# Performance work log

Hardware: AMD Instinct MI355X
Metric: run time of the kernel (lower is better)

## Reference

```python
import jax, jax.numpy as jnp
import numpy as np

B, C, D, H, W = 4, 256, 16, 16, 16


def setup_inputs() -> dict:
    key = jax.random.key(0)
    ks = jax.random.split(key, 9)
    s = 1.0 / np.sqrt(C)
    inp = {
        "x": jax.random.normal(ks[0], (B, C, D, H, W), dtype=jnp.float32),
        "wq": jax.random.normal(ks[1], (C, C), dtype=jnp.float32) * s,
        "bq": jax.random.normal(ks[2], (C,), dtype=jnp.float32) * 0.02,
        "wk": jax.random.normal(ks[3], (C, C), dtype=jnp.float32) * s,
        "bk": jax.random.normal(ks[4], (C,), dtype=jnp.float32) * 0.02,
        "wv": jax.random.normal(ks[5], (C, C), dtype=jnp.float32) * s,
        "bv": jax.random.normal(ks[6], (C,), dtype=jnp.float32) * 0.02,
        "wp": jax.random.normal(ks[7], (C, C), dtype=jnp.float32) * s,
        "bp": jax.random.normal(ks[8], (C,), dtype=jnp.float32) * 0.02,
    }
    return inp


def reference(x, wq, bq, wk, bk, wv, bv, wp, bp):
    b, c, d, h, w = x.shape
    xf = x.reshape(b, c, d * h * w)  # (B, C, N)
    # 1x1 Conv3d == per-voxel linear map over channels
    q = jnp.einsum('oc,bcn->bon', wq, xf) + bq[:, None]
    k = jnp.einsum('oc,bcn->bon', wk, xf) + bk[:, None]
    v = jnp.einsum('oc,bcn->bon', wv, xf) + bv[:, None]
    # scores[b,i,j] = q[:, :, i] . k[:, :, j], scaled AFTER the bmm (as in source)
    scores = jnp.einsum('bci,bcj->bij', q, k) * (c ** -0.5)
    p = jax.nn.softmax(scores, axis=2)  # (B, N, N), softmax over keys j
    # attention[b,c,i] = sum_j v[b,c,j] * p[b,i,j]
    attn = jnp.einsum('bcj,bij->bci', v, p)
    out = jnp.einsum('oc,bcn->bon', wp, attn) + bp[:, None]
    return x + out.reshape(b, c, d, h, w)
```

## Files before the change

kernel.cpp:

```cpp
#include <hip/hip_runtime.h>

typedef unsigned short u16;
typedef unsigned int u32;
typedef __bf16 v8bf __attribute__((ext_vector_type(8)));
typedef float v4f __attribute__((ext_vector_type(4)));

#define DEV __device__ __forceinline__

constexpr int CB = 4;
constexpr int C = 256;
constexpr int NN = 4096;
constexpr float LOG2E = 1.4426950408889634f;
constexpr int PST = 44;

DEV u16 f2bf(float f) {
  union { float f; u32 u; } v; v.f = f;
  u32 r = v.u + 0x7fffu + ((v.u >> 16) & 1u);
  return (u16)(r >> 16);
}
DEV float bf2f(u16 h) {
  union { u32 u; float f; } v; v.u = ((u32)h) << 16; return v.f;
}

DEV void dma16(const u16* g, const u16* lds_base) {
  __builtin_amdgcn_global_load_lds(
      (const __attribute__((address_space(1))) void*)(unsigned long long)g,
      (__attribute__((address_space(3))) void*)(u32)(unsigned long long)lds_base,
      16, 0, 0);
}

__global__ __launch_bounds__(256) void k_transpose(const float* __restrict__ x,
                                                   u16* __restrict__ xT) {
  __shared__ float tile[32][33];
  int b = blockIdx.z;
  int n0 = blockIdx.x * 32, c0 = blockIdx.y * 32;
  int tx = threadIdx.x & 31, ty = threadIdx.x >> 5;
  const float* xb = x + (long)b * C * NN;
#pragma unroll
  for (int r = 0; r < 4; ++r)
    tile[ty + r * 8][tx] = xb[(long)(c0 + ty + r * 8) * NN + n0 + tx];
  __syncthreads();
  u16* xTb = xT + (long)b * NN * C;
#pragma unroll
  for (int r = 0; r < 4; ++r)
    xTb[(long)(n0 + ty + r * 8) * C + c0 + tx] = f2bf(tile[tx][ty + r * 8]);
}

__global__ __launch_bounds__(256) void k_cvt4(const float* __restrict__ s0,
                                              const float* __restrict__ s1,
                                              const float* __restrict__ s2,
                                              const float* __restrict__ s3,
                                              u16* __restrict__ d0, u16* __restrict__ d1,
                                              u16* __restrict__ d2, u16* __restrict__ d3,
                                              float* __restrict__ Mbuf) {
  if (blockIdx.x == 0 && blockIdx.y == 0 && threadIdx.x < 8) Mbuf[threadIdx.x] = 0.f;
  int wsel = blockIdx.y;
  const float* s = wsel == 0 ? s0 : wsel == 1 ? s1 : wsel == 2 ? s2 : s3;
  u16* d = wsel == 0 ? d0 : wsel == 1 ? d1 : wsel == 2 ? d2 : d3;
  int i = blockIdx.x * 256 + threadIdx.x;
  d[i] = f2bf(s[i]);
}

DEV void stage_dma(const u16* __restrict__ g, const u16* lds, int w, int lane) {
#pragma unroll
  for (int i = 0; i < 8; ++i) {
    int idx = w * 8 + i;
    int r = idx * 2 + (lane >> 5);
    int cg = (lane & 31) ^ (r & 7);
    dma16(g + (long)r * 256 + cg * 8, lds + idx * 512);
  }
}

__global__ __launch_bounds__(256) void k_qkv(
    const u16* __restrict__ xT, const u16* __restrict__ wqb, const u16* __restrict__ wkb,
    const u16* __restrict__ wvb, const float* __restrict__ bq, const float* __restrict__ bk,
    const float* __restrict__ bv, u16* __restrict__ qO, u16* __restrict__ kO,
    u16* __restrict__ vO) {
  __shared__ __align__(16) u16 Ash[64 * 256];
  __shared__ __align__(16) u16 Bsh[64 * 256];
  int t = threadIdx.x, w = t >> 6, lane = t & 63, lr = lane & 15, q = lane >> 4;
  int m0 = blockIdx.x * 64, n0 = blockIdx.y * 64, b = blockIdx.z;
  const int xk = lr & 7;
  stage_dma(xT + (long)b * NN * C + (long)m0 * 256, Ash, w, lane);
  stage_dma(wqb + (long)n0 * 256, Bsh, w, lane);
  asm volatile("s_waitcnt vmcnt(0)\n\ts_barrier" ::: "memory");
#pragma unroll 1
  for (int wsel = 0; wsel < 3; ++wsel) {
    v4f acc[4];
#pragma unroll
    for (int nt = 0; nt < 4; ++nt)
#pragma unroll
      for (int r = 0; r < 4; ++r) acc[nt][r] = 0.f;
#pragma unroll
    for (int ks = 0; ks < 8; ++ks) {
      int cg = ((ks * 4 + q) ^ xk) << 3;
      v8bf a = *reinterpret_cast<const v8bf*>(Ash + (w * 16 + lr) * 256 + cg);
#pragma unroll
      for (int nt = 0; nt < 4; ++nt) {
        v8bf bb = *reinterpret_cast<const v8bf*>(Bsh + (nt * 16 + lr) * 256 + cg);
        acc[nt] = __builtin_amdgcn_mfma_f32_16x16x32_bf16(a, bb, acc[nt], 0, 0, 0);
      }
    }
    asm volatile("s_waitcnt lgkmcnt(0)\n\ts_barrier" ::: "memory");
    if (wsel < 2) {
      stage_dma((wsel == 0 ? wkb : wvb) + (long)n0 * 256, Bsh, w, lane);
      const float* bias = wsel == 0 ? bq : bk;
#pragma unroll
      for (int nt = 0; nt < 4; ++nt) {
#pragma unroll
        for (int r = 0; r < 4; ++r) {
          int gm = m0 + w * 16 + q * 4 + r;
          int gn = n0 + nt * 16 + lr;
          float val = acc[nt][r] + bias[gn];
          if (wsel == 0) {
            qO[((long)b * NN + gm) * C + gn] = f2bf(val * (0.0625f * LOG2E));
          } else {
            kO[((long)b * NN + gm) * C + gn] = f2bf(val);
          }
        }
      }
      asm volatile("s_waitcnt vmcnt(0)\n\ts_barrier" ::: "memory");
    } else {
      u16* Vt = Ash;
#pragma unroll
      for (int nt = 0; nt < 4; ++nt) {
#pragma unroll
        for (int r = 0; r < 4; ++r) {
          int gn_l = nt * 16 + lr;
          int gm_l = w * 16 + q * 4 + r;
          float val = acc[nt][r] + bv[n0 + gn_l];
          Vt[gn_l * 72 + gm_l] = f2bf(val);
        }
      }
      asm volatile("s_waitcnt lgkmcnt(0)\n\ts_barrier" ::: "memory");
      int row = t >> 2;
      u16* vrow = vO + (long)b * C * NN + (long)(n0 + row) * NN + m0;
#pragma unroll
      for (int s2 = 0; s2 < 2; ++s2) {
        int seg = (t & 3) * 2 + s2;
        *reinterpret_cast<uint4*>(vrow + seg * 8) =
            *reinterpret_cast<const uint4*>(Vt + row * 72 + seg * 8);
      }
    }
  }
}

__global__ __launch_bounds__(256) void k_maxnorm(const u16* __restrict__ qT,
                                                 const u16* __restrict__ kT,
                                                 float* __restrict__ Mbuf) {
  int b = blockIdx.z, tsel = blockIdx.y;
  const u16* src = (tsel ? kT : qT) + (long)b * NN * C;
  int row = blockIdx.x * 64 + (threadIdx.x >> 2);
  const uint4* pp =
      reinterpret_cast<const uint4*>(src + (long)row * C + (threadIdx.x & 3) * 64);
  float s = 0.f;
#pragma unroll
  for (int u = 0; u < 8; ++u) {
    uint4 d = pp[u];
    const u16* e = reinterpret_cast<const u16*>(&d);
#pragma unroll
    for (int i = 0; i < 8; ++i) { float f = bf2f(e[i]); s += f * f; }
  }
  s += __shfl_xor(s, 1, 64);
  s += __shfl_xor(s, 2, 64);
#pragma unroll
  for (int d2 = 4; d2 < 64; d2 <<= 1) s = fmaxf(s, __shfl_xor(s, d2, 64));
  if ((threadIdx.x & 63) == 0)
    atomicMax((u32*)(Mbuf + tsel * 4 + b), __float_as_uint(s));
}

__global__ __launch_bounds__(256) void k_gemm(
    const u16* __restrict__ A, long aStr, const u16* __restrict__ Bm, long bStr,
    const float* __restrict__ biasM, const float* __restrict__ biasN,
    const float* __restrict__ resid, long rStr, float scale,
    float* __restrict__ outF, u16* __restrict__ outH, long oStr, int ldm, int ldn) {
  __shared__ __align__(16) u16 Ash[64 * 256];
  __shared__ __align__(16) u16 Bsh[64 * 256];
  int t = threadIdx.x;
  int w = t >> 6, lane = t & 63, lr = lane & 15, q = lane >> 4;
  int m0 = blockIdx.x * 64, n0 = blockIdx.y * 64, b = blockIdx.z;
  const int xk = lr & 7;
  stage_dma(A + b * aStr + (long)m0 * 256, Ash, w, lane);
  stage_dma(Bm + b * bStr + (long)n0 * 256, Bsh, w, lane);
  asm volatile("s_waitcnt vmcnt(0)\n\ts_barrier" ::: "memory");
  v4f acc[4];
#pragma unroll
  for (int nt = 0; nt < 4; ++nt)
#pragma unroll
    for (int r = 0; r < 4; ++r) acc[nt][r] = 0.f;
#pragma unroll
  for (int ks = 0; ks < 8; ++ks) {
    int cg = ((ks * 4 + q) ^ xk) << 3;
    v8bf a = *reinterpret_cast<const v8bf*>(Ash + (w * 16 + lr) * 256 + cg);
#pragma unroll
    for (int nt = 0; nt < 4; ++nt) {
      v8bf bb = *reinterpret_cast<const v8bf*>(Bsh + (nt * 16 + lr) * 256 + cg);
      acc[nt] = __builtin_amdgcn_mfma_f32_16x16x32_bf16(a, bb, acc[nt], 0, 0, 0);
    }
  }
#pragma unroll
  for (int nt = 0; nt < 4; ++nt) {
#pragma unroll
    for (int r = 0; r < 4; ++r) {
      int gm = m0 + w * 16 + q * 4 + r;
      int gn = n0 + nt * 16 + lr;
      float val = acc[nt][r];
      if (biasM) val += biasM[gm];
      if (biasN) val += biasN[gn];
      val *= scale;
      long addr = b * oStr + (long)gm * ldm + (long)gn * ldn;
      if (resid) val += resid[b * rStr + (long)gm * ldm + (long)gn * ldn];
      if (outF) outF[addr] = val;
      else outH[addr] = f2bf(val);
    }
  }
}

DEV void flash_issue(const u16* kb, const u16* vb, const u16* kshb, const u16* vshb,
                     int j0, int w, int lane) {
#pragma unroll
  for (int i = 0; i < 4; ++i) {
    int idx = w * 4 + i;
    int kr = idx * 2 + (lane >> 5);
    int kc = (lane & 31) ^ (kr & 7);
    dma16(kb + (long)(j0 + kr) * 256 + kc * 8, kshb + idx * 512);
  }
#pragma unroll
  for (int i = 0; i < 4; ++i) {
    int idx = w * 4 + i;
    int vr = idx * 16 + (lane >> 2);
    int vc = (lane & 3) ^ ((vr ^ (vr >> 2)) & 3);
    dma16(vb + (long)vr * NN + j0 + vc * 8, vshb + idx * 512);
  }
}

__global__ __launch_bounds__(256, 2) void k_flash(const u16* __restrict__ qT,
                                                  const u16* __restrict__ kT,
                                                  const u16* __restrict__ V,
                                                  u16* __restrict__ op0,
                                                  u16* __restrict__ op1,
                                                  u16* __restrict__ op2,
                                                  u16* __restrict__ op3,
                                                  float* __restrict__ ml,
                                                  const float* __restrict__ Mbuf,
                                                  int span) {
  __shared__ __align__(16) u16 ksh[2][32 * 256];
  __shared__ __align__(16) u16 vsh[2][256 * 32];
  __shared__ __align__(16) u16 psh[64 * PST];
  int t = threadIdx.x;
  int w = t >> 6, lane = t & 63, lr = lane & 15, q = lane >> 4;
  int b = blockIdx.z, h = blockIdx.y;
  int i0 = blockIdx.x * 64;
  const u16* qb = qT + ((long)b * NN + i0 + w * 16) * C;
  const u16* kb = kT + (long)b * NN * C;
  const u16* vb = V + (long)b * C * NN;
  float M = sqrtf(Mbuf[b] * Mbuf[4 + b]) + 1.0f;

  v8bf qf[8];
#pragma unroll
  for (int ks = 0; ks < 8; ++ks)
    qf[ks] = *reinterpret_cast<const v8bf*>(qb + lr * C + ks * 32 + q * 8);

  v4f accO[16];
#pragma unroll
  for (int ct = 0; ct < 16; ++ct)
#pragma unroll
    for (int r = 0; r < 4; ++r) accO[ct][r] = 0.f;
  float lsum[4] = {0.f, 0.f, 0.f, 0.f};

  u16* pw = psh + w * 16 * PST;
  const int xk = lr & 7;
  const int xv = (lr ^ (lr >> 2)) & 3;

  int jstart = h * span;
  int niter = span >> 5;
  flash_issue(kb, vb, ksh[0], vsh[0], jstart, w, lane);
  int cur = 0;
#pragma unroll 1
  for (int it = 0; it < niter; ++it) {
    int j0 = jstart + (it << 5);
    int jn = (it + 1 < niter) ? j0 + 32 : jstart;
    asm volatile("s_waitcnt lgkmcnt(0)\n\ts_barrier" ::: "memory");
    flash_issue(kb, vb, ksh[cur ^ 1], vsh[cur ^ 1], jn, w, lane);
    asm volatile("s_waitcnt vmcnt(8)\n\ts_barrier" ::: "memory");

    const u16* kcur = ksh[cur];
    const u16* vcur = vsh[cur];
    v4f s[2];
#pragma unroll
    for (int jt = 0; jt < 2; ++jt)
#pragma unroll
      for (int r = 0; r < 4; ++r) s[jt][r] = 0.f;
#pragma unroll
    for (int ks = 0; ks < 8; ++ks) {
#pragma unroll
      for (int jt = 0; jt < 2; ++jt) {
        v8bf kf = *reinterpret_cast<const v8bf*>(
            kcur + (jt * 16 + lr) * 256 + (((ks * 4 + q) ^ xk) << 3));
        s[jt] = __builtin_amdgcn_mfma_f32_16x16x32_bf16(qf[ks], kf, s[jt], 0, 0, 0);
      }
    }

#pragma unroll
    for (int jt = 0; jt < 2; ++jt) {
#pragma unroll
      for (int r = 0; r < 4; ++r) {
        float p = exp2f(s[jt][r] - M);
        lsum[r] += p;
        u32 pb = (__float_as_uint(p) + 0x8000u) >> 16;
        pw[(q * 4 + r) * PST + jt * 16 + lr] = (u16)pb;
      }
    }
    asm volatile("s_waitcnt lgkmcnt(0)\n\ts_barrier" ::: "memory");
    v8bf pa[4];
#pragma unroll
    for (int qs = 0; qs < 4; ++qs)
      pa[qs] = *reinterpret_cast<const v8bf*>(psh + (qs * 16 + lr) * PST + q * 8);
    const u16* vwp = vcur + w * 64 * 32;
#pragma unroll
    for (int cs = 0; cs < 4; ++cs) {
      v8bf v0 = *reinterpret_cast<const v8bf*>(
          vwp + (cs * 16 + lr) * 32 + ((q ^ xv) << 3));
#pragma unroll
      for (int qs = 0; qs < 4; ++qs)
        accO[qs * 4 + cs] =
            __builtin_amdgcn_mfma_f32_16x16x32_bf16(pa[qs], v0, accO[qs * 4 + cs], 0, 0, 0);
    }
    cur ^= 1;
  }

#pragma unroll
  for (int r = 0; r < 4; ++r) {
#pragma unroll
    for (int d = 1; d < 16; d <<= 1) lsum[r] += __shfl_xor(lsum[r], d, 64);
  }
  u16* opp = h == 0 ? op0 : h == 1 ? op1 : h == 2 ? op2 : op3;
  u16* ob = opp + ((long)b * NN + i0) * C;
#pragma unroll
  for (int qs = 0; qs < 4; ++qs)
#pragma unroll
    for (int cs = 0; cs < 4; ++cs)
#pragma unroll
      for (int r = 0; r < 4; ++r)
        ob[(qs * 16 + q * 4 + r) * C + w * 64 + cs * 16 + lr] =
            f2bf(accO[qs * 4 + cs][r]);
  if (lr == 0) {
    long rbase = ((long)h * CB + b) * NN + i0 + w * 16 + q * 4;
#pragma unroll
    for (int r = 0; r < 4; ++r) {
      ml[(rbase + r) * 2] = M;
      ml[(rbase + r) * 2 + 1] = lsum[r];
    }
  }
}

__global__ __launch_bounds__(256) void k_combine(const u16* __restrict__ p0,
                                                 const u16* __restrict__ p1,
                                                 const u16* __restrict__ p2,
                                                 const u16* __restrict__ p3,
                                                 const float* __restrict__ ml,
                                                 u16* __restrict__ o, int js) {
  long row = (long)blockIdx.x * 8 + (threadIdx.x >> 5);
  int tc = (threadIdx.x & 31) * 8;
  float m[4], l[4];
  float mx = -3.0e38f;
  for (int h = 0; h < js; ++h) {
    m[h] = ml[((long)h * CB * NN + row) * 2];
    l[h] = ml[((long)h * CB * NN + row) * 2 + 1];
    mx = fmaxf(mx, m[h]);
  }
  float tot = 0.f, a[4];
  for (int h = 0; h < js; ++h) { a[h] = exp2f(m[h] - mx); tot += a[h] * l[h]; }
  float inv = 1.f / tot;
  float acc[8];
#pragma unroll
  for (int i = 0; i < 8; ++i) acc[i] = 0.f;
  const u16* ps[4] = {p0, p1, p2, p3};
  for (int h = 0; h < js; ++h) {
    uint4 u = *reinterpret_cast<const uint4*>(ps[h] + row * C + tc);
    const u16* p = reinterpret_cast<const u16*>(&u);
    float wgt = a[h] * inv;
#pragma unroll
    for (int i = 0; i < 8; ++i) acc[i] += wgt * bf2f(p[i]);
  }
  u16 outv[8];
#pragma unroll
  for (int i = 0; i < 8; ++i) outv[i] = f2bf(acc[i]);
  *reinterpret_cast<uint4*>(o + row * C + tc) = *reinterpret_cast<const uint4*>(outv);
}

extern "C" void kernel_launch(void* const* d_in, const int* in_sizes, int n_in,
                              void* d_out, int out_size, void* d_ws, size_t ws_size,
                              hipStream_t stream) {
  const float* x = (const float*)d_in[0];
  const float* wq = (const float*)d_in[1];
  const float* bq = (const float*)d_in[2];
  const float* wk = (const float*)d_in[3];
  const float* bk = (const float*)d_in[4];
  const float* wv = (const float*)d_in[5];
  const float* bv = (const float*)d_in[6];
  const float* wp = (const float*)d_in[7];
  const float* bp = (const float*)d_in[8];
  float* out = (float*)d_out;
  char* ws = (char*)d_ws;

  const long SLOT = 8388608L;
  const size_t NEED4 = 524288UL + 7 * 8388608UL + 524288UL + 4096UL;
  int js = (ws_size >= NEED4) ? 4 : 2;

  u16* wqb = (u16*)(ws + 0);
  u16* wkb = (u16*)(ws + 131072L);
  u16* wvb = (u16*)(ws + 262144L);
  u16* wpb = (u16*)(ws + 393216L);
  char* base = ws + 524288L;
  u16* xT  = (u16*)(base);
  u16* qTw = (u16*)(base + 1 * SLOT);
  u16* kTw = (u16*)(base + 2 * SLOT);
  u16* vw  = (u16*)(base + 3 * SLOT);
  u16* op1 = (u16*)(base + 4 * SLOT);
  u16* op2 = js == 4 ? (u16*)(base + 5 * SLOT) : op1;
  u16* op3 = js == 4 ? (u16*)(base + 6 * SLOT) : op1;
  float* ml = (float*)(base + (js == 4 ? 7 : 5) * SLOT);
  float* Mbuf = ml + 131072;
  u16* op0 = xT;
  u16* oW  = qTw;

  k_cvt4<<<dim3(256, 4), 256, 0, stream>>>(wq, wk, wv, wp, wqb, wkb, wvb, wpb, Mbuf);
  k_transpose<<<dim3(128, 8, CB), 256, 0, stream>>>(x, xT);
  k_qkv<<<dim3(64, 4, CB), 256, 0, stream>>>(xT, wqb, wkb, wvb, bq, bk, bv, qTw, kTw, vw);
  k_maxnorm<<<dim3(64, 2, CB), 256, 0, stream>>>(qTw, kTw, Mbuf);
  k_flash<<<dim3(64, js, CB), 256, 0, stream>>>(qTw, kTw, vw, op0, op1, op2, op3, ml,
                                                Mbuf, NN / js);
  k_combine<<<2048, 256, 0, stream>>>(op0, op1, op2, op3, ml, oW, js);

  long nc = (long)NN * C;
  k_gemm<<<dim3(4, 64, CB), 256, 0, stream>>>(wpb, 0, oW, nc, bp, nullptr, x, nc,
                                              1.0f, out, nullptr, nc, NN, 1);
}
```

Baseline: 265.0 us.

## Software-pipeline flash loop: V in registers, double-buffered P, one barrier per step

Restructures the attention inner loop so V tiles are loaded directly from global memory into registers instead of staged through LDS. P is double-buffered in shared memory so the PV MFMA for iteration it-1 overlaps with the QK and softmax of iteration it. Only one barrier remains per step, and the loop is manually unrolled by two to alternate buffers. This cuts LDS traffic and synchronisation, but raises register pressure and relies on an even iteration count.

```diff
diff --git a/kernel.cpp b/kernel.cpp
--- a/kernel.cpp
+++ b/kernel.cpp
@@ -216,8 +216,7 @@
   }
 }
 
-DEV void flash_issue(const u16* kb, const u16* vb, const u16* kshb, const u16* vshb,
-                     int j0, int w, int lane) {
+DEV void kissue(const u16* kb, const u16* kshb, int j0, int w, int lane) {
 #pragma unroll
   for (int i = 0; i < 4; ++i) {
     int idx = w * 4 + i;
@@ -225,14 +224,48 @@
     int kc = (lane & 31) ^ (kr & 7);
     dma16(kb + (long)(j0 + kr) * 256 + kc * 8, kshb + idx * 512);
   }
-#pragma unroll
-  for (int i = 0; i < 4; ++i) {
-    int idx = w * 4 + i;
-    int vr = idx * 16 + (lane >> 2);
-    int vc = (lane & 3) ^ ((vr ^ (vr >> 2)) & 3);
-    dma16(vb + (long)vr * NN + j0 + vc * 8, vshb + idx * 512);
-  }
-}
+}
+
+#define FLASH_STEP(IT, VL, VU, PW, PR, KC, KN)                                     \
+  {                                                                                \
+    int jn_ = ((IT) + 1 < niter) ? jstart + (((IT) + 1) << 5) : jstart;            \
+    kissue(kb, (KN), jn_, w, lane);                                                \
+    asm volatile("" ::: "memory");    \
+    {                                                                              \
+      int jv_ = jstart + ((IT) << 5);                                              \
+      _Pragma("unroll") for (int cs = 0; cs < 4; ++cs)                             \
+          VL[cs] = *reinterpret_cast<const v8bf*>(                                 \
+              vbw + (long)(cs * 16 + lr) * NN + jv_ + q * 8);                      \
+    }                                                                              \
+    v4f s0_, s1_;                                                                  \
+    _Pragma("unroll") for (int r = 0; r < 4; ++r) { s0_[r] = 0.f; s1_[r] = 0.f; }  \
+    _Pragma("unroll") for (int ks = 0; ks < 8; ++ks) {                             \
+      int cg_ = ((ks * 4 + q) ^ xk) << 3;                                          \
+      v8bf k0_ = *reinterpret_cast<const v8bf*>((KC) + lr * 256 + cg_);            \
+      v8bf k1_ = *reinterpret_cast<const v8bf*>((KC) + (16 + lr) * 256 + cg_);     \
+      s0_ = __builtin_amdgcn_mfma_f32_16x16x32_bf16(qf[ks], k0_, s0_, 0, 0, 0);    \
+      s1_ = __builtin_amdgcn_mfma_f32_16x16x32_bf16(qf[ks], k1_, s1_, 0, 0, 0);    \
+    }                                                                              \
+    _Pragma("unroll") for (int r = 0; r < 4; ++r) {                                \
+      float p0_ = exp2f(s0_[r] - M);                                               \
+      float p1_ = exp2f(s1_[r] - M);                                               \
+      lsum[r] += p0_ + p1_;                                                        \
+      (PW)[(q * 4 + r) * PST + lr] = (u16)((__float_as_uint(p0_) + 0x8000u) >> 16);\
+      (PW)[(q * 4 + r) * PST + 16 + lr] =                                          \
+          (u16)((__float_as_uint(p1_) + 0x8000u) >> 16);                           \
+    }                                                                              \
+    if ((IT) > 0) {                                                                \
+      v8bf pa_[4];                                                                 \
+      _Pragma("unroll") for (int qs = 0; qs < 4; ++qs)                             \
+          pa_[qs] = *reinterpret_cast<const v8bf*>(                                \
+              (PR) + (qs * 16 + lr) * PST + q * 8);                                \
+      _Pragma("unroll") for (int cs = 0; cs < 4; ++cs)                             \
+        _Pragma("unroll") for (int qs = 0; qs < 4; ++qs)                           \
+          accO[qs * 4 + cs] = __builtin_amdgcn_mfma_f32_16x16x32_bf16(             \
+              pa_[qs], VU[cs], accO[qs * 4 + cs], 0, 0, 0);                        \
+    }                                                                              \
+    asm volatile("s_waitcnt vmcnt(4) lgkmcnt(0)\n\ts_barrier" ::: "memory");       \
+  }
 
 __global__ __launch_bounds__(256, 2) void k_flash(const u16* __restrict__ qT,
                                                   const u16* __restrict__ kT,
@@ -245,15 +278,14 @@
                                                   const float* __restrict__ Mbuf,
                                                   int span) {
   __shared__ __align__(16) u16 ksh[2][32 * 256];
-  __shared__ __align__(16) u16 vsh[2][256 * 32];
-  __shared__ __align__(16) u16 psh[64 * PST];
+  __shared__ __align__(16) u16 psh[2][64 * PST];
   int t = threadIdx.x;
   int w = t >> 6, lane = t & 63, lr = lane & 15, q = lane >> 4;
   int b = blockIdx.z, h = blockIdx.y;
   int i0 = blockIdx.x * 64;
   const u16* qb = qT + ((long)b * NN + i0 + w * 16) * C;
   const u16* kb = kT + (long)b * NN * C;
-  const u16* vb = V + (long)b * C * NN;
+  const u16* vbw = V + (long)b * C * NN + (long)(w * 64) * NN;
   float M = sqrtf(Mbuf[b] * Mbuf[4 + b]) + 1.0f;
 
   v8bf qf[8];
@@ -268,65 +300,33 @@
     for (int r = 0; r < 4; ++r) accO[ct][r] = 0.f;
   float lsum[4] = {0.f, 0.f, 0.f, 0.f};
 
-  u16* pw = psh + w * 16 * PST;
+  u16* pw0 = psh[0] + w * 16 * PST;
+  u16* pw1 = psh[1] + w * 16 * PST;
   const int xk = lr & 7;
-  const int xv = (lr ^ (lr >> 2)) & 3;
 
   int jstart = h * span;
   int niter = span >> 5;
-  flash_issue(kb, vb, ksh[0], vsh[0], jstart, w, lane);
-  int cur = 0;
+
+  kissue(kb, ksh[0], jstart, w, lane);
+  asm volatile("s_waitcnt vmcnt(0)\n\ts_barrier" ::: "memory");
+
+  v8bf vA[4] = {}, vB[4] = {};
 #pragma unroll 1
-  for (int it = 0; it < niter; ++it) {
-    int j0 = jstart + (it << 5);
-    int jn = (it + 1 < niter) ? j0 + 32 : jstart;
-    asm volatile("s_waitcnt lgkmcnt(0)\n\ts_barrier" ::: "memory");
-    flash_issue(kb, vb, ksh[cur ^ 1], vsh[cur ^ 1], jn, w, lane);
-    asm volatile("s_waitcnt vmcnt(8)\n\ts_barrier" ::: "memory");
-
-    const u16* kcur = ksh[cur];
-    const u16* vcur = vsh[cur];
-    v4f s[2];
-#pragma unroll
-    for (int jt = 0; jt < 2; ++jt)
-#pragma unroll
-      for (int r = 0; r < 4; ++r) s[jt][r] = 0.f;
-#pragma unroll
-    for (int ks = 0; ks < 8; ++ks) {
-#pragma unroll
-      for (int jt = 0; jt < 2; ++jt) {
-        v8bf kf = *reinterpret_cast<const v8bf*>(
-            kcur + (jt * 16 + lr) * 256 + (((ks * 4 + q) ^ xk) << 3));
-        s[jt] = __builtin_amdgcn_mfma_f32_16x16x32_bf16(qf[ks], kf, s[jt], 0, 0, 0);
-      }
-    }
-
-#pragma unroll
-    for (int jt = 0; jt < 2; ++jt) {
-#pragma unroll
-      for (int r = 0; r < 4; ++r) {
-        float p = exp2f(s[jt][r] - M);
-        lsum[r] += p;
-        u32 pb = (__float_as_uint(p) + 0x8000u) >> 16;
-        pw[(q * 4 + r) * PST + jt * 16 + lr] = (u16)pb;
-      }
-    }
-    asm volatile("s_waitcnt lgkmcnt(0)\n\ts_barrier" ::: "memory");
-    v8bf pa[4];
+  for (int it2 = 0; it2 < niter; it2 += 2) {
+    FLASH_STEP(it2,     vA, vB, pw0, psh[1], ksh[0], ksh[1])
+    FLASH_STEP(it2 + 1, vB, vA, pw1, psh[0], ksh[1], ksh[0])
+  }
+  {
+    v8bf pa_[4];
 #pragma unroll
     for (int qs = 0; qs < 4; ++qs)
-      pa[qs] = *reinterpret_cast<const v8bf*>(psh + (qs * 16 + lr) * PST + q * 8);
-    const u16* vwp = vcur + w * 64 * 32;
-#pragma unroll
-    for (int cs = 0; cs < 4; ++cs) {
-      v8bf v0 = *reinterpret_cast<const v8bf*>(
-          vwp + (cs * 16 + lr) * 32 + ((q ^ xv) << 3));
+      pa_[qs] = *reinterpret_cast<const v8bf*>(psh[1] + (qs * 16 + lr) * PST + q * 8);
+#pragma unroll
+    for (int cs = 0; cs < 4; ++cs)
 #pragma unroll
       for (int qs = 0; qs < 4; ++qs)
-        accO[qs * 4 + cs] =
-            __builtin_amdgcn_mfma_f32_16x16x32_bf16(pa[qs], v0, accO[qs * 4 + cs], 0, 0, 0);
-    }
-    cur ^= 1;
+        accO[qs * 4 + cs] = __builtin_amdgcn_mfma_f32_16x16x32_bf16(
+            pa_[qs], vB[cs], accO[qs * 4 + cs], 0, 0, 0);
   }
 
 #pragma unroll
```

After: 267.9 us. About the same (+1.1%).
